# Kernel tuning notes

Hardware: AMD Instinct MI355X
Metric: run time of the kernel (lower is better)

Reference implementation:

```python
import jax, jax.numpy as jnp
import numpy as np

SAMPLE_SIZE = 8192
K = 8
N_SPLATS = 1_000_000
EPS = 1e-12  # keeps sqrt grad finite on zero-distance (duplicate) pairs


def setup_inputs() -> dict:
    key = jax.random.key(0)
    k1, k2, k3 = jax.random.split(key, 3)
    means = jax.random.normal(k1, (N_SPLATS, 3), dtype=jnp.float32)
    sh0 = jax.random.normal(k2, (N_SPLATS, 1, 3), dtype=jnp.float32)
    idx = jax.random.randint(k3, (SAMPLE_SIZE,), 0, N_SPLATS, dtype=jnp.int64)
    return {"means": means, "sh0": sh0, "idx": idx}


def reference(means, sh0, idx):
    sh0 = sh0.squeeze(1)                    # [N, 3]
    sm = means[idx]                         # [S, 3] sampled positions
    ss = sh0[idx]                           # [S, 3] sampled colors
    # pairwise euclidean distances (torch.cdist, p=2): [S, S]
    sq = jnp.sum(sm * sm, axis=-1)
    d2 = sq[:, None] + sq[None, :] - 2.0 * (sm @ sm.T)
    dist = jnp.sqrt(jnp.maximum(d2, EPS))
    # k+1 smallest per row; drop self (column 0)
    _, knn_idx = jax.lax.top_k(-dist, K + 1)           # [S, K+1]
    knn_idx = knn_idx[:, 1:]                           # [S, K]
    neighbors_sh0 = ss[knn_idx]                        # [S, K, 3]
    neighbor_dist = jnp.take_along_axis(dist, knn_idx, axis=1)[..., None]  # [S, K, 1]
    weight = jnp.exp(-neighbor_dist)
    diff = ss[:, None, :] - neighbors_sh0              # [S, K, 3]
    return jnp.mean(weight * diff * diff)
```

## Files before the change

kernel.cpp:

```cpp
#include <hip/hip_runtime.h>
#include <float.h>
#include <math.h>

#define NSAMPLE 8192
#define KSEL 9
#define KNN 8
#define BLK 512
#define EPS_F 1e-12f

#define ROWS_PB 8
#define NBLOCKS (NSAMPLE / ROWS_PB)
#define RPT 8
#define LANES 64
#define KQT 16
#define BNDI 4
#define WCAP 32
#define BP 129
#define IDX_MASK 0x1FFFu
#define VAL_MASK 0xFFFFE000u
#define PROW 73
#define SROW 145
#define SCALE (1.0f / (float)(NSAMPLE * KNN * 3))

__device__ __forceinline__ unsigned umn(unsigned a, unsigned b) { return a < b ? a : b; }
__device__ __forceinline__ unsigned umx(unsigned a, unsigned b) { return a > b ? a : b; }

__device__ __forceinline__ void insert9(unsigned s[KSEL], unsigned x)
{
#pragma unroll
    for (int k = 0; k < KSEL - 1; ++k)
        s[k] = umx(s[k + 1], umn(x, s[k]));
    s[KSEL - 1] = umn(x, s[KSEL - 1]);
}

__device__ __forceinline__ unsigned pack_d2(float d2, int gidx)
{
    return (__float_as_uint(fmaxf(d2, 0.0f)) & VAL_MASK) | (unsigned)gidx;
}

__device__ __forceinline__ float sfl(float x)
{
    return __uint_as_float((unsigned)__builtin_amdgcn_readfirstlane(
        (int)__float_as_uint(x)));
}

__device__ __forceinline__ unsigned mbcnt64(unsigned long long m)
{
    return __builtin_amdgcn_mbcnt_hi((unsigned)(m >> 32),
           __builtin_amdgcn_mbcnt_lo((unsigned)(m & 0xFFFFFFFFull), 0u));
}

__global__ __launch_bounds__(256) void gather_k(
    const float* __restrict__ means, const float* __restrict__ sh0,
    const int* __restrict__ idx,
    float4* __restrict__ sm4, float4* __restrict__ ss4)
{
    int i = blockIdx.x * 256 + threadIdx.x;
    if (i >= NSAMPLE) return;
    int id = idx[i];
    const float* m = means + 3 * id;
    const float* s = sh0 + 3 * id;
    float mx = m[0], my = m[1], mz = m[2];
    sm4[i] = make_float4(mx, my, mz, fmaf(mx, mx, fmaf(my, my, mz * mz)));
    ss4[i] = make_float4(s[0], s[1], s[2], 0.0f);
}

#define QUAD(R, Q, CI)                                                        \
    {                                                                         \
        float v0 = fmaf(cX[(R) + 0], (Q).x, fmaf(cY[(R) + 0], (Q).y,          \
                   fmaf(cZ[(R) + 0], (Q).z, (Q).w)));                         \
        float v1 = fmaf(cX[(R) + 1], (Q).x, fmaf(cY[(R) + 1], (Q).y,          \
                   fmaf(cZ[(R) + 1], (Q).z, (Q).w)));                         \
        float v2 = fmaf(cX[(R) + 2], (Q).x, fmaf(cY[(R) + 2], (Q).y,          \
                   fmaf(cZ[(R) + 2], (Q).z, (Q).w)));                         \
        float v3 = fmaf(cX[(R) + 3], (Q).x, fmaf(cY[(R) + 3], (Q).y,          \
                   fmaf(cZ[(R) + 3], (Q).z, (Q).w)));                         \
        unsigned long long m0 = __ballot(v0 <= sb[(R) + 0]);                  \
        unsigned long long m1 = __ballot(v1 <= sb[(R) + 1]);                  \
        unsigned long long m2 = __ballot(v2 <= sb[(R) + 2]);                  \
        unsigned long long m3 = __ballot(v3 <= sb[(R) + 3]);                  \
        if (m0) {                                                             \
            unsigned pos = base[(R) + 0] + mbcnt64(m0);                       \
            if ((v0 <= sb[(R) + 0]) && pos < WCAP)                            \
                wl[(w * RPT + (R) + 0) * WCAP + pos] =                        \
                    pack_d2(v0 + cW[(R) + 0], (CI));                          \
            base[(R) + 0] += (unsigned)__popcll(m0);                          \
        }                                                                     \
        if (m1) {                                                             \
            unsigned pos = base[(R) + 1] + mbcnt64(m1);                       \
            if ((v1 <= sb[(R) + 1]) && pos < WCAP)                            \
                wl[(w * RPT + (R) + 1) * WCAP + pos] =                        \
                    pack_d2(v1 + cW[(R) + 1], (CI));                          \
            base[(R) + 1] += (unsigned)__popcll(m1);                          \
        }                                                                     \
        if (m2) {                                                             \
            unsigned pos = base[(R) + 2] + mbcnt64(m2);                       \
            if ((v2 <= sb[(R) + 2]) && pos < WCAP)                            \
                wl[(w * RPT + (R) + 2) * WCAP + pos] =                        \
                    pack_d2(v2 + cW[(R) + 2], (CI));                          \
            base[(R) + 2] += (unsigned)__popcll(m2);                          \
        }                                                                     \
        if (m3) {                                                             \
            unsigned pos = base[(R) + 3] + mbcnt64(m3);                       \
            if ((v3 <= sb[(R) + 3]) && pos < WCAP)                            \
                wl[(w * RPT + (R) + 3) * WCAP + pos] =                        \
                    pack_d2(v3 + cW[(R) + 3], (CI));                          \
            base[(R) + 3] += (unsigned)__popcll(m3);                          \
        }                                                                     \
    }

__global__ __launch_bounds__(BLK, 6) void main_k(
    const float4* __restrict__ sm4, const float4* __restrict__ ss4,
    float* __restrict__ partial)
{
    __shared__ unsigned wl[8 * RPT * WCAP];
    __shared__ unsigned wcnt[8 * RPT];
    __shared__ unsigned bpart[ROWS_PB * BP];
    __shared__ unsigned scratch[ROWS_PB * SROW];
    __shared__ unsigned partS[ROWS_PB * PROW];
    __shared__ unsigned bnd[ROWS_PB];
    __shared__ float    red[ROWS_PB];

    const int t = threadIdx.x;
    const int lane = t & (LANES - 1);
    const int w = t >> 6;

    float cX[RPT], cY[RPT], cZ[RPT], cW[RPT];
#pragma unroll
    for (int i = 0; i < RPT; ++i) {
        float4 p = sm4[blockIdx.x * ROWS_PB + i];
        cX[i] = sfl(-2.0f * p.x);
        cY[i] = sfl(-2.0f * p.y);
        cZ[i] = sfl(-2.0f * p.z);
        cW[i] = sfl(p.w);
    }

    {
        unsigned pm[RPT];
#pragma unroll
        for (int i = 0; i < RPT; ++i) pm[i] = 0xFFFFFFFFu;
        const int b0 = w * (KQT * LANES);
#pragma unroll
        for (int k = 0; k < BNDI; ++k) {
            const int ci = b0 + k * LANES + lane;
            float4 q = sm4[ci];
#pragma unroll
            for (int i = 0; i < RPT; ++i) {
                float s = fmaf(cX[i], q.x,
                          fmaf(cY[i], q.y, fmaf(cZ[i], q.z, q.w)));
                pm[i] = umn(pm[i], pack_d2(s + cW[i], ci));
            }
        }
#pragma unroll
        for (int i = 0; i < RPT; ++i) {
            pm[i] = umn(pm[i], (unsigned)__shfl_xor((int)pm[i], 32, 64));
            pm[i] = umn(pm[i], (unsigned)__shfl_xor((int)pm[i], 16, 64));
        }
        if (lane < 16) {
#pragma unroll
            for (int i = 0; i < RPT; ++i)
                bpart[i * BP + w * 16 + lane] = pm[i];
        }
    }
    __syncthreads();

    if (t < 128) {
        const int r1 = t & (ROWS_PB - 1);
        const int g = t >> 3;
        unsigned s[KSEL];
#pragma unroll
        for (int k = 0; k < KSEL; ++k) s[k] = 0xFFFFFFFFu;
#pragma unroll
        for (int e = 0; e < 8; ++e)
            insert9(s, bpart[r1 * BP + g * 8 + e]);
#pragma unroll
        for (int k = 0; k < KSEL; ++k)
            scratch[r1 * SROW + g * KSEL + k] = s[k];
    }
    __syncthreads();
    if (t < 64) {
        const int r1 = t & (ROWS_PB - 1);
        const int mg = t >> 3;
        unsigned m[KSEL];
#pragma unroll
        for (int k = 0; k < KSEL; ++k) m[k] = 0xFFFFFFFFu;
#pragma unroll
        for (int e = 0; e < 2 * KSEL; ++e)
            insert9(m, scratch[r1 * SROW + (2 * mg) * KSEL + e]);
#pragma unroll
        for (int k = 0; k < KSEL; ++k)
            partS[r1 * PROW + mg * KSEL + k] = m[k];
    }
    __syncthreads();
    if (t < ROWS_PB) {
        unsigned m[KSEL];
#pragma unroll
        for (int k = 0; k < KSEL; ++k) m[k] = 0xFFFFFFFFu;
#pragma unroll
        for (int e = 0; e < 8 * KSEL; ++e)
            insert9(m, partS[t * PROW + e]);
        bnd[t] = m[0];
    }
    __syncthreads();

    float sb[RPT];
#pragma unroll
    for (int i = 0; i < RPT; ++i) {
        float bfv = __uint_as_float(bnd[i] | IDX_MASK);
        float D = bfv - cW[i];
        sb[i] = sfl(D + (bfv + fabsf(D)) * 6.0e-7f + 1e-33f);
    }

    unsigned base[RPT];
#pragma unroll
    for (int i = 0; i < RPT; ++i) base[i] = 0u;

    const int s0 = w * (KQT * LANES);
    const float4* __restrict__ qp = sm4 + s0 + lane;

    float4 qa = qp[0];
#pragma unroll 1
    for (int k0 = 0; k0 < KQT; k0 += 2) {
        float4 qb = qp[(k0 + 1) * LANES];
        {
            const int ci = s0 + k0 * LANES + lane;
            QUAD(0, qa, ci)
            QUAD(4, qa, ci)
        }
        qa = qp[(k0 + 2) * LANES];
        {
            const int ci = s0 + (k0 + 1) * LANES + lane;
            QUAD(0, qb, ci)
            QUAD(4, qb, ci)
        }
    }
    if (lane == 0) {
#pragma unroll
        for (int i = 0; i < RPT; ++i)
            wcnt[w * RPT + i] = umn(base[i], WCAP);
    }
    __syncthreads();

    if (t < 64) {
        const int r1 = t & (ROWS_PB - 1);
        const int wv = t >> 3;
        const int li = wv * RPT + r1;
        const unsigned n = wcnt[li];
        unsigned s[KSEL];
#pragma unroll
        for (int k = 0; k < KSEL; ++k) s[k] = 0xFFFFFFFFu;
        for (unsigned k = 0; k < n; ++k)
            insert9(s, wl[li * WCAP + k]);
#pragma unroll
        for (int k = 0; k < KSEL; ++k)
            partS[r1 * PROW + wv * KSEL + k] = s[k];
    }
    __syncthreads();

    if (t < ROWS_PB) {
        unsigned m[KSEL];
#pragma unroll
        for (int k = 0; k < KSEL; ++k) m[k] = 0xFFFFFFFFu;
#pragma unroll
        for (int e = 0; e < 8 * KSEL; ++e)
            insert9(m, partS[t * PROW + e]);

        const int gr = blockIdx.x * ROWS_PB + t;
        float4 pm4 = sm4[gr];
        float4 ps4 = ss4[gr];
        float acc = 0.0f;
#pragma unroll
        for (int k = 0; k < KNN; ++k) {
            int j = (int)(m[k] & IDX_MASK);
            float4 qm = sm4[j];
            float dx = pm4.x - qm.x, dy = pm4.y - qm.y, dz = pm4.z - qm.z;
            float d2 = fmaf(dx, dx, fmaf(dy, dy, dz * dz));
            float d = sqrtf(fmaxf(d2, EPS_F));
            float wgt = expf(-d);
            float4 qs = ss4[j];
            float ax = ps4.x - qs.x, ay = ps4.y - qs.y, az = ps4.z - qs.z;
            acc += wgt * (ax * ax + ay * ay + az * az);
        }
        red[t] = acc;
    }
    __syncthreads();
    if (t == 0) {
        float ssum = 0.0f;
#pragma unroll
        for (int i = 0; i < ROWS_PB; ++i) ssum += red[i];
        partial[blockIdx.x] = ssum;
    }
}

__global__ __launch_bounds__(256) void reduce_k(
    const float* __restrict__ partial, float* __restrict__ out)
{
    __shared__ float sbuf[4];
    int t = threadIdx.x;
    float v = 0.0f;
    for (int i = t; i < NBLOCKS; i += 256) v += partial[i];
    for (int off = 32; off > 0; off >>= 1) v += __shfl_down(v, off);
    if ((t & 63) == 0) sbuf[t >> 6] = v;
    __syncthreads();
    if (t == 0) {
        float s = sbuf[0] + sbuf[1] + sbuf[2] + sbuf[3];
        out[0] = s * SCALE;
    }
}

extern "C" void kernel_launch(void* const* d_in, const int* in_sizes, int n_in,
                              void* d_out, int out_size, void* d_ws, size_t ws_size,
                              hipStream_t stream)
{
    const float* means = (const float*)d_in[0];
    const float* sh0   = (const float*)d_in[1];
    const int*   idxp  = (const int*)d_in[2];

    float4* sm4 = (float4*)d_ws;
    float4* ss4 = sm4 + NSAMPLE;
    float*  partial = (float*)(ss4 + NSAMPLE);

    gather_k<<<NSAMPLE / 256, 256, 0, stream>>>(means, sh0, idxp, sm4, ss4);
    main_k<<<NBLOCKS, BLK, 0, stream>>>(sm4, ss4, partial);
    reduce_k<<<1, 256, 0, stream>>>(partial, (float*)d_out);
}
```

Measured before the change: 98.11 us.

## Stage candidate points through LDS with async global_load_lds double buffering

The main scan loop now copies candidate point chunks straight from global memory into a per-wave double-buffered LDS staging area using global_load_lds, prefetching the next chunk while the current one is processed. Before, each float4 was loaded into registers with a one-step software prefetch. The aim is to hide global load latency and lower register pressure. The cost is extra LDS space, which can reduce occupancy, plus LDS reads. The last iteration prefetches one chunk past the wave's range, which may read beyond the buffer on the final wave.

```diff
diff --git a/kernel.cpp b/kernel.cpp
--- a/kernel.cpp
+++ b/kernel.cpp
@@ -13,6 +13,8 @@
 #define RPT 8
 #define LANES 64
 #define KQT 16
+#define CHUNK 128
+#define NCHUNK (1024 / CHUNK)
 #define BNDI 4
 #define WCAP 32
 #define BP 129
@@ -48,6 +50,13 @@
 {
     return __builtin_amdgcn_mbcnt_hi((unsigned)(m >> 32),
            __builtin_amdgcn_mbcnt_lo((unsigned)(m & 0xFFFFFFFFull), 0u));
+}
+
+__device__ __forceinline__ void load_lds16(const float4* g, float4* l)
+{
+    __builtin_amdgcn_global_load_lds(
+        (const __attribute__((address_space(1))) void*)g,
+        (__attribute__((address_space(3))) void*)l, 16, 0, 0);
 }
 
 __global__ __launch_bounds__(256) void gather_k(
@@ -113,6 +122,7 @@
     const float4* __restrict__ sm4, const float4* __restrict__ ss4,
     float* __restrict__ partial)
 {
+    __shared__ float4   stg[8][2][CHUNK];
     __shared__ unsigned wl[8 * RPT * WCAP];
     __shared__ unsigned wcnt[8 * RPT];
     __shared__ unsigned bpart[ROWS_PB * BP];
@@ -140,10 +150,11 @@
 #pragma unroll
         for (int i = 0; i < RPT; ++i) pm[i] = 0xFFFFFFFFu;
         const int b0 = w * (KQT * LANES);
+        const float4* __restrict__ bp = sm4 + b0 + lane;
 #pragma unroll
         for (int k = 0; k < BNDI; ++k) {
             const int ci = b0 + k * LANES + lane;
-            float4 q = sm4[ci];
+            float4 q = bp[k * LANES];
 #pragma unroll
             for (int i = 0; i < RPT; ++i) {
                 float s = fmaf(cX[i], q.x,
@@ -216,24 +227,31 @@
     for (int i = 0; i < RPT; ++i) base[i] = 0u;
 
     const int s0 = w * (KQT * LANES);
-    const float4* __restrict__ qp = sm4 + s0 + lane;
-
-    float4 qa = qp[0];
+    const float4* __restrict__ gsrc = sm4 + s0;
+
+    load_lds16(gsrc + lane,      &stg[w][0][0]);
+    load_lds16(gsrc + 64 + lane, &stg[w][0][64]);
+
 #pragma unroll 1
-    for (int k0 = 0; k0 < KQT; k0 += 2) {
-        float4 qb = qp[(k0 + 1) * LANES];
-        {
-            const int ci = s0 + k0 * LANES + lane;
-            QUAD(0, qa, ci)
-            QUAD(4, qa, ci)
-        }
-        qa = qp[(k0 + 2) * LANES];
-        {
-            const int ci = s0 + (k0 + 1) * LANES + lane;
-            QUAD(0, qb, ci)
-            QUAD(4, qb, ci)
-        }
-    }
+    for (int c = 0; c < NCHUNK; ++c) {
+        const float4* gn = gsrc + (c + 1) * CHUNK;
+        float4* ln = &stg[w][(c + 1) & 1][0];
+        load_lds16(gn + lane,      ln);
+        load_lds16(gn + 64 + lane, ln + 64);
+
+        asm volatile("s_waitcnt vmcnt(2)" ::: "memory");
+        __builtin_amdgcn_sched_barrier(0);
+
+        const float4* buf = &stg[w][c & 1][0];
+        float4 q0 = buf[lane];
+        float4 q1 = buf[64 + lane];
+        const int ci0 = s0 + c * CHUNK + lane;
+        QUAD(0, q0, ci0)
+        QUAD(4, q0, ci0)
+        QUAD(0, q1, ci0 + 64)
+        QUAD(4, q1, ci0 + 64)
+    }
+
     if (lane == 0) {
 #pragma unroll
         for (int i = 0; i < RPT; ++i)
```

Result: slower. 106.7 us (+8.8%).
